# Optimization experiments

Measured on AMD Instinct MI355X. Metric: run time of the kernel, lower is better.

## Reference

```python
import jax, jax.numpy as jnp
import numpy as np

NUM_NODES = 100000
HIDDEN = 128
OFFSET = 2  # GNNEmbedding.OFFSET


def gcn_conv(x, src, dst, W, b, n):
    # GCNConv: D^{-1/2} (A + I) D^{-1/2} X W + b, with self-loops added
    loops = jnp.arange(n)
    s = jnp.concatenate([src, loops])
    d = jnp.concatenate([dst, loops])
    deg = jax.ops.segment_sum(jnp.ones(s.shape, x.dtype), d, num_segments=n)
    dinv = jax.lax.rsqrt(jnp.maximum(deg, 1e-12))
    norm = dinv[s] * dinv[d]          # [E+n]
    msg = x[s] * norm[:, None]        # [E+n, H]  dominant memory traffic
    agg = jax.ops.segment_sum(msg, d, num_segments=n)
    return agg @ W + b


def setup_inputs():
    key = jax.random.key(0)
    ks = jax.random.split(key, 8)
    E = 1_600_000
    B, S = 16, 2048
    src = jax.random.randint(ks[0], (E,), 0, NUM_NODES)
    dst = jax.random.randint(ks[1], (E,), 0, NUM_NODES)
    ei = jnp.stack([src, dst])
    seq = jax.random.randint(ks[2], (B, S), 0, NUM_NODES)
    specials = jax.random.randint(ks[3], (B, S), -2, 20)
    seq = jnp.where(specials < 0, specials, seq)
    emb = jax.random.normal(ks[4], (NUM_NODES + 2, HIDDEN), jnp.float32) * 0.02
    lim = 1.0 / np.sqrt(HIDDEN)
    W0 = jax.random.uniform(ks[5], (HIDDEN, HIDDEN), jnp.float32, -lim, lim)
    W1 = jax.random.uniform(ks[6], (HIDDEN, HIDDEN), jnp.float32, -lim, lim)
    b0 = jnp.zeros((HIDDEN,), jnp.float32)
    b1 = jnp.zeros((HIDDEN,), jnp.float32)
    return {"emb": emb, "W0": W0, "b0": b0, "W1": W1, "b1": b1,
            "ei": ei, "seq": seq}


def reference(emb, W0, b0, W1, b1, ei, seq):
    src, dst = ei[0], ei[1]
    x = emb[:NUM_NODES]                               # embedding(arange(num_nodes))
    h = jax.nn.relu(gcn_conv(x, src, dst, W0, b0, NUM_NODES))
    z = gcn_conv(h, src, dst, W1, b1, NUM_NODES)      # no act on last GCN layer
    nodes = seq >= 0
    node_idx = jnp.where(nodes, seq, 0)
    spec_idx = jnp.where(nodes, 0, seq + OFFSET + NUM_NODES)
    # embs[nodes] = z[seq[nodes]]; embs[~nodes] = emb[seq+OFFSET+num_nodes]
    embs = jnp.where(nodes[..., None], z[node_idx], emb[spec_idx])
    return embs
```

## Files before the change

kernel.cpp:

```cpp
#include <hip/hip_runtime.h>

#define HDIM 128
#define OFF_SPECIAL 2
#define BSTRIDE 48

typedef __attribute__((ext_vector_type(8))) short bf16x8;
typedef __attribute__((ext_vector_type(4))) float f32x4;
typedef __attribute__((ext_vector_type(2))) float f32x2;

__device__ __forceinline__ float bf2f(unsigned short u) {
    union { unsigned int i; float f; } v;
    v.i = ((unsigned int)u) << 16;
    return v.f;
}
__device__ __forceinline__ unsigned short f2bf(float f) {
    union { float f; unsigned int i; } v;
    v.f = f;
    unsigned int x = v.i;
    x += 0x7FFFu + ((x >> 16) & 1u);
    return (unsigned short)(x >> 16);
}

#define XSCALE 16.0f
#define XINV   0.0625f

#define SEG 500
#define PSTRIDE 48
#define PART_W 256
#define CAST_BLOCKS 512
#define FLAG_BLOCKS 16

__global__ void k_part(const int* __restrict__ src, const int* __restrict__ dst,
                       int E, unsigned int* __restrict__ partbuf,
                       int* __restrict__ cntAB, int partN,
                       const float* __restrict__ emb,
                       unsigned char* __restrict__ embf8, int n4,
                       const int* __restrict__ seqp, int P,
                       unsigned char* __restrict__ flag) {
    __shared__ int lcnt[SEG];
    int tid = threadIdx.x;
    if (blockIdx.x < PART_W) {
        for (int i = tid; i < SEG; i += 256) lcnt[i] = 0;
        __syncthreads();
        int w = blockIdx.x;
        int chunk = (E + PART_W - 1) / PART_W;
        int e0 = w * chunk;
        int e1 = e0 + chunk; if (e1 > E) e1 = E;
        for (int e = e0 + tid; e < e1; e += 256) {
            int d = dst[e];
            int s = src[e];
            int seg = d / partN;
            int dloc = d - seg * partN;
            unsigned int pack = (unsigned int)s | ((unsigned int)dloc << 17);
            int slot = atomicAdd(&lcnt[seg], 1);
            if (slot < PSTRIDE)
                partbuf[((size_t)seg * PART_W + w) * PSTRIDE + slot] = pack;
        }
        __syncthreads();
        for (int i = tid; i < SEG; i += 256) {
            int c = lcnt[i];
            cntAB[i * PART_W + w] = c < PSTRIDE ? c : PSTRIDE;
        }
    } else if (blockIdx.x < PART_W + CAST_BLOCKS) {
        int i0 = (blockIdx.x - PART_W) * 256 + tid;
        for (int i = i0; i < n4; i += CAST_BLOCKS * 256) {
            float4 v = ((const float4*)emb)[i];
            int lo = __builtin_amdgcn_cvt_pk_fp8_f32(v.x * XSCALE, v.y * XSCALE, 0, false);
            int pk = __builtin_amdgcn_cvt_pk_fp8_f32(v.z * XSCALE, v.w * XSCALE, lo, true);
            ((int*)embf8)[i] = pk;
        }
    } else {
        int i0 = (blockIdx.x - PART_W - CAST_BLOCKS) * 256 + tid;
        for (int p = i0; p < P; p += FLAG_BLOCKS * 256) {
            int sv = seqp[p];
            if (sv >= 0) flag[sv] = 1;
        }
    }
}

__global__ void k_place(const unsigned int* __restrict__ partbuf,
                        const int* __restrict__ cntAB,
                        int* __restrict__ adjB, int* __restrict__ cnt,
                        float* __restrict__ dinv, int partN, int N) {
    __shared__ int lcur[256];
    int tid = threadIdx.x;
    int s = blockIdx.x;
    for (int i = tid; i < partN; i += 256) lcur[i] = 0;
    __syncthreads();
    int g = tid >> 4;
    int l16 = tid & 15;
    int cpre = cntAB[s * PART_W + g + 16 * l16];
    const unsigned int* segbuf = partbuf + (size_t)s * PART_W * PSTRIDE;
#pragma unroll 4
    for (int k = 0; k < 16; ++k) {
        int c = __shfl(cpre, k, 16);
        int w = g + 16 * k;
        const unsigned int* sb = segbuf + w * PSTRIDE;
        for (int idx = l16; idx < c; idx += 16) {
            unsigned int v = sb[idx];
            int sv = (int)(v & 0x1FFFFu);
            int dloc = (int)(v >> 17);
            int slot = atomicAdd(&lcur[dloc], 1);
            if (slot < BSTRIDE)
                adjB[((size_t)s * partN + dloc) * BSTRIDE + slot] = sv;
        }
    }
    __syncthreads();
    for (int i = tid; i < partN; i += 256) {
        int d = s * partN + i;
        if (d < N) {
            int c = lcur[i];
            cnt[d] = c;
            dinv[d] = rsqrtf((float)c + 1.0f);
        }
    }
}

template <int FP8, int SPARSE>
__global__ __launch_bounds__(256, 8) void k_pull(
        const void* __restrict__ xv, const int* __restrict__ cnt,
        const int* __restrict__ adjB, const float* __restrict__ dinv,
        unsigned short* __restrict__ agg, int N,
        const unsigned char* __restrict__ flag) {
    int row = blockIdx.x * 4 + (threadIdx.x >> 6);
    if (row >= N) return;
    if (SPARSE && !flag[row]) return;
    int lane = threadIdx.x & 63;
    int d = cnt[row];
    if (d > BSTRIDE) d = BSTRIDE;
    const int* nbr = adjB + (size_t)row * BSTRIDE;
    float dr = dinv[row];
    const unsigned char* x8 = (const unsigned char*)xv;
    unsigned int boff = FP8 ? 2u * (unsigned int)lane : 4u * (unsigned int)lane;
    unsigned int rstr = FP8 ? HDIM : HDIM * 2;

    float ax, ay;
    {
        float sc = dr * dr;
        float vx, vy;
        if (FP8) {
            unsigned int p = *(const unsigned short*)(x8 + (size_t)(unsigned)row * rstr + boff);
            f32x2 f = __builtin_amdgcn_cvt_pk_f32_fp8((int)p, false);
            vx = f.x; vy = f.y;
        } else {
            unsigned int u = *(const unsigned int*)(x8 + (size_t)(unsigned)row * rstr + boff);
            vx = bf2f((unsigned short)u); vy = bf2f((unsigned short)(u >> 16));
        }
        ax = vx * sc; ay = vy * sc;
    }
    int t = 0;
    for (; t + 8 <= d; t += 8) {
        int4 q0 = *(const int4*)(nbr + t);
        int4 q1 = *(const int4*)(nbr + t + 4);
        int s[8] = {q0.x, q0.y, q0.z, q0.w, q1.x, q1.y, q1.z, q1.w};
        float nr[8];
        unsigned int u[8];
#pragma unroll
        for (int i = 0; i < 8; ++i) {
            nr[i] = dinv[s[i]] * dr;
            if (FP8) u[i] = *(const unsigned short*)(x8 + (size_t)(unsigned)s[i] * rstr + boff);
            else     u[i] = *(const unsigned int*)(x8 + (size_t)(unsigned)s[i] * rstr + boff);
        }
#pragma unroll
        for (int i = 0; i < 8; ++i) {
            float vx, vy;
            if (FP8) {
                f32x2 f = __builtin_amdgcn_cvt_pk_f32_fp8((int)u[i], false);
                vx = f.x; vy = f.y;
            } else {
                vx = bf2f((unsigned short)u[i]); vy = bf2f((unsigned short)(u[i] >> 16));
            }
            ax = fmaf(vx, nr[i], ax);
            ay = fmaf(vy, nr[i], ay);
        }
    }
    if (t + 4 <= d) {
        int4 q0 = *(const int4*)(nbr + t);
        int s[4] = {q0.x, q0.y, q0.z, q0.w};
        float nr[4];
        unsigned int u[4];
#pragma unroll
        for (int i = 0; i < 4; ++i) {
            nr[i] = dinv[s[i]] * dr;
            if (FP8) u[i] = *(const unsigned short*)(x8 + (size_t)(unsigned)s[i] * rstr + boff);
            else     u[i] = *(const unsigned int*)(x8 + (size_t)(unsigned)s[i] * rstr + boff);
        }
#pragma unroll
        for (int i = 0; i < 4; ++i) {
            float vx, vy;
            if (FP8) {
                f32x2 f = __builtin_amdgcn_cvt_pk_f32_fp8((int)u[i], false);
                vx = f.x; vy = f.y;
            } else {
                vx = bf2f((unsigned short)u[i]); vy = bf2f((unsigned short)(u[i] >> 16));
            }
            ax = fmaf(vx, nr[i], ax);
            ay = fmaf(vy, nr[i], ay);
        }
        t += 4;
    }
    for (; t < d; ++t) {
        int s = nbr[t];
        float nr = dinv[s] * dr;
        float vx, vy;
        if (FP8) {
            unsigned int p = *(const unsigned short*)(x8 + (size_t)(unsigned)s * rstr + boff);
            f32x2 f = __builtin_amdgcn_cvt_pk_f32_fp8((int)p, false);
            vx = f.x; vy = f.y;
        } else {
            unsigned int u = *(const unsigned int*)(x8 + (size_t)(unsigned)s * rstr + boff);
            vx = bf2f((unsigned short)u); vy = bf2f((unsigned short)(u >> 16));
        }
        ax = fmaf(vx, nr, ax);
        ay = fmaf(vy, nr, ay);
    }
    unsigned int pack = (unsigned int)f2bf(ax) | ((unsigned int)f2bf(ay) << 16);
    *(unsigned int*)(agg + (size_t)(unsigned)row * HDIM + 2u * (unsigned int)lane) = pack;
}

template <int RELU, int SPARSE>
__global__ __launch_bounds__(256) void k_gemm_mfma(
        const unsigned short* __restrict__ A, const float* __restrict__ W,
        const float* __restrict__ bias, float bscale,
        unsigned short* __restrict__ out, int N,
        const unsigned char* __restrict__ flag) {
    __shared__ __align__(16) unsigned short Wt[HDIM * 136];
    int tid = threadIdx.x;
    for (int i = tid; i < HDIM * HDIM; i += 256) {
        int k = i >> 7, n = i & 127;
        Wt[n * 136 + k] = f2bf(W[i]);
    }
    int lane = tid & 63;
    int wv = tid >> 6;
    int n15 = lane & 15, q = lane >> 4;
    float bv[8];
#pragma unroll
    for (int ct = 0; ct < 8; ++ct) bv[ct] = bscale * bias[ct * 16 + n15];
    __syncthreads();

    int nChunks = (N + 63) / 64;
    for (int c = blockIdx.x; c < nChunks; c += gridDim.x) {
        int row0 = c * 64 + wv * 16;
        if (SPARSE) {
            int frow = row0 + n15;
            int fl = (frow < N) ? flag[frow] : 0;
            if (__ballot(fl != 0) == 0ULL) continue;
        }
        const unsigned short* arow = A + (size_t)(row0 + n15) * HDIM + q * 8;
        bf16x8 a0 = *(const bf16x8*)(arow);
        bf16x8 a1 = *(const bf16x8*)(arow + 32);
        bf16x8 a2 = *(const bf16x8*)(arow + 64);
        bf16x8 a3 = *(const bf16x8*)(arow + 96);
#pragma unroll
        for (int ct = 0; ct < 8; ++ct) {
            const unsigned short* wrow = &Wt[(ct * 16 + n15) * 136 + q * 8];
            f32x4 acc = {0.f, 0.f, 0.f, 0.f};
            acc = __builtin_amdgcn_mfma_f32_16x16x32_bf16(a0, *(const bf16x8*)(wrow),      acc, 0, 0, 0);
            acc = __builtin_amdgcn_mfma_f32_16x16x32_bf16(a1, *(const bf16x8*)(wrow + 32), acc, 0, 0, 0);
            acc = __builtin_amdgcn_mfma_f32_16x16x32_bf16(a2, *(const bf16x8*)(wrow + 64), acc, 0, 0, 0);
            acc = __builtin_amdgcn_mfma_f32_16x16x32_bf16(a3, *(const bf16x8*)(wrow + 96), acc, 0, 0, 0);
#pragma unroll
            for (int r = 0; r < 4; ++r) {
                int row = row0 + q * 4 + r;
                if (row < N && (!SPARSE || flag[row])) {
                    float v = acc[r] + bv[ct];
                    if (RELU) v = fmaxf(v, 0.0f);
                    out[(size_t)row * HDIM + ct * 16 + n15] = f2bf(v);
                }
            }
        }
    }
}

__global__ void k_gather(const int* __restrict__ seq, int P,
                         const unsigned short* __restrict__ z,
                         const float* __restrict__ emb, int N,
                         float* __restrict__ out) {
    int gid = blockIdx.x * blockDim.x + threadIdx.x;
    int p = gid >> 5, c = gid & 31;
    if (p >= P) return;
    int sv = seq[p];
    float4 v;
    if (sv >= 0) {
        uint2 u = *(const uint2*)(z + (size_t)sv * HDIM + c * 4);
        v = make_float4(bf2f((unsigned short)u.x) * XINV,
                        bf2f((unsigned short)(u.x >> 16)) * XINV,
                        bf2f((unsigned short)u.y) * XINV,
                        bf2f((unsigned short)(u.y >> 16)) * XINV);
    } else {
        v = *(const float4*)(emb + (size_t)(sv + OFF_SPECIAL + N) * HDIM + c * 4);
    }
    *(float4*)(out + (size_t)p * HDIM + c * 4) = v;
}

extern "C" void kernel_launch(void* const* d_in, const int* in_sizes, int n_in,
                              void* d_out, int out_size, void* d_ws, size_t ws_size,
                              hipStream_t stream) {
    const float* emb = (const float*)d_in[0];
    const float* W0  = (const float*)d_in[1];
    const float* b0  = (const float*)d_in[2];
    const float* W1  = (const float*)d_in[3];
    const float* b1  = (const float*)d_in[4];
    const int* ei  = (const int*)d_in[5];
    const int* seq = (const int*)d_in[6];

    int N = in_sizes[0] / HDIM - OFF_SPECIAL;
    int E = in_sizes[5] / 2;
    int P = in_sizes[6];
    const int* srcp = ei;
    const int* dstp = ei + E;

    char* ws = (char*)d_ws;
    size_t off = 0;
    auto alloc = [&](size_t bytes) {
        void* p = ws + off;
        off = (off + bytes + 255) & ~(size_t)255;
        return p;
    };
    unsigned short* aggbf = (unsigned short*)alloc((size_t)N * HDIM * sizeof(unsigned short));
    unsigned short* buf1  = (unsigned short*)alloc((size_t)N * HDIM * sizeof(unsigned short));
    int*   adjB = (int*)alloc((size_t)N * BSTRIDE * sizeof(int));
    int*   cnt  = (int*)alloc((size_t)N * sizeof(int));
    unsigned char* flag = (unsigned char*)alloc((size_t)N);
    float* dinv = (float*)alloc((size_t)N * sizeof(float));
    unsigned int* partbuf = (unsigned int*)aggbf;
    unsigned char* embf8  = (unsigned char*)buf1;
    int* cntAB = (int*)((char*)buf1 + 16u * 1024u * 1024u);

    hipMemsetAsync(flag, 0, (size_t)N, stream);

    int partN = (N + SEG - 1) / SEG;
    int n4 = N * HDIM / 4;
    k_part<<<PART_W + CAST_BLOCKS + FLAG_BLOCKS, 256, 0, stream>>>(
        srcp, dstp, E, partbuf, cntAB, partN, emb, embf8, n4, seq, P, flag);
    k_place<<<SEG, 256, 0, stream>>>(partbuf, cntAB, adjB, cnt, dinv, partN, N);

    int pullBlocks = (N + 3) / 4;

    k_pull<1, 0><<<pullBlocks, 256, 0, stream>>>(embf8, cnt, adjB, dinv, aggbf, N, nullptr);
    k_gemm_mfma<1, 0><<<640, 256, 0, stream>>>(aggbf, W0, b0, XSCALE, buf1, N, nullptr);

    k_pull<0, 1><<<pullBlocks, 256, 0, stream>>>(buf1, cnt, adjB, dinv, aggbf, N, flag);
    k_gemm_mfma<0, 1><<<640, 256, 0, stream>>>(aggbf, W1, b1, XSCALE, aggbf, N, flag);

    k_gather<<<(P * 32 + 255) / 256, 256, 0, stream>>>(seq, P, aggbf, emb, N,
                                                       (float*)d_out);
}
```

Baseline: 307.2 us.

## Fuse first-layer neighbor aggregation with MFMA GEMM and fold flag memset into partition kernel

Adds a k_conv kernel that aggregates 64 rows per block into LDS and then multiplies them by a bf16 copy of W0 with MFMA, with bias and ReLU, in the same kernel. This drops the intermediate aggregation buffer write and read, plus one launch, for layer one. The flag memset moves into k_part, and the flag scatter moves into extra blocks of k_place to remove a separate memset call. The risk is that every block now converts the whole W into LDS, and the fused kernel's large LDS use and 16 serial rows per wave may lower occupancy and latency hiding compared with the separate pull kernel.

New measurement: 384.7 us. 1.25x slower.

```diff
diff --git a/kernel.cpp b/kernel.cpp
--- a/kernel.cpp
+++ b/kernel.cpp
@@ -35,8 +35,7 @@
                        int* __restrict__ cntAB, int partN,
                        const float* __restrict__ emb,
                        unsigned char* __restrict__ embf8, int n4,
-                       const int* __restrict__ seqp, int P,
-                       unsigned char* __restrict__ flag) {
+                       unsigned char* __restrict__ flag, int N) {
     __shared__ int lcnt[SEG];
     int tid = threadIdx.x;
     if (blockIdx.x < PART_W) {
@@ -71,19 +70,31 @@
         }
     } else {
         int i0 = (blockIdx.x - PART_W - CAST_BLOCKS) * 256 + tid;
+        int n16 = N >> 4;
+        for (int i = i0; i < n16; i += FLAG_BLOCKS * 256) {
+            ((int4*)flag)[i] = make_int4(0, 0, 0, 0);
+        }
+        if (blockIdx.x == PART_W + CAST_BLOCKS && tid < (N & 15))
+            flag[(n16 << 4) + tid] = 0;
+    }
+}
+
+__global__ void k_place(const unsigned int* __restrict__ partbuf,
+                        const int* __restrict__ cntAB,
+                        int* __restrict__ adjB, int* __restrict__ cnt,
+                        float* __restrict__ dinv, int partN, int N,
+                        const int* __restrict__ seqp, int P,
+                        unsigned char* __restrict__ flag) {
+    __shared__ int lcur[256];
+    int tid = threadIdx.x;
+    if (blockIdx.x >= SEG) {
+        int i0 = (blockIdx.x - SEG) * 256 + tid;
         for (int p = i0; p < P; p += FLAG_BLOCKS * 256) {
             int sv = seqp[p];
             if (sv >= 0) flag[sv] = 1;
         }
-    }
-}
-
-__global__ void k_place(const unsigned int* __restrict__ partbuf,
-                        const int* __restrict__ cntAB,
-                        int* __restrict__ adjB, int* __restrict__ cnt,
-                        float* __restrict__ dinv, int partN, int N) {
-    __shared__ int lcur[256];
-    int tid = threadIdx.x;
+        return;
+    }
     int s = blockIdx.x;
     for (int i = tid; i < partN; i += 256) lcur[i] = 0;
     __syncthreads();
@@ -116,6 +127,152 @@
     }
 }
 
+template <int FP8, int RELU, int SPARSE>
+__global__ __launch_bounds__(256) void k_conv(
+        const void* __restrict__ xv, const int* __restrict__ cnt,
+        const int* __restrict__ adjB, const float* __restrict__ dinv,
+        const float* __restrict__ W, const float* __restrict__ bias, float bscale,
+        unsigned short* __restrict__ out, int N,
+        const unsigned char* __restrict__ flag) {
+    __shared__ __align__(16) unsigned short Wt[HDIM * 136];
+    __shared__ __align__(16) unsigned short aggT[64 * 136];
+    int tid = threadIdx.x;
+    for (int i = tid; i < HDIM * HDIM; i += 256) {
+        int k = i >> 7, n = i & 127;
+        Wt[n * 136 + k] = f2bf(W[i]);
+    }
+    int lane = tid & 63;
+    int wv = tid >> 6;
+    int n15 = lane & 15, q = lane >> 4;
+    float bv[8];
+#pragma unroll
+    for (int ct = 0; ct < 8; ++ct) bv[ct] = bscale * bias[ct * 16 + n15];
+
+    int row0 = blockIdx.x * 64;
+    const unsigned char* x8 = (const unsigned char*)xv;
+    unsigned int boff = FP8 ? 2u * (unsigned int)lane : 4u * (unsigned int)lane;
+    unsigned int rstr = FP8 ? HDIM : HDIM * 2;
+
+    for (int rr = 0; rr < 16; ++rr) {
+        int lr = wv * 16 + rr;
+        int row = row0 + lr;
+        if (row >= N) break;
+        if (SPARSE && !flag[row]) continue;
+        int d = cnt[row];
+        if (d > BSTRIDE) d = BSTRIDE;
+        const int* nbr = adjB + (size_t)row * BSTRIDE;
+        float dr = dinv[row];
+
+        float ax, ay;
+        {
+            float sc = dr * dr;
+            float vx, vy;
+            if (FP8) {
+                unsigned int p = *(const unsigned short*)(x8 + (size_t)(unsigned)row * rstr + boff);
+                f32x2 f = __builtin_amdgcn_cvt_pk_f32_fp8((int)p, false);
+                vx = f.x; vy = f.y;
+            } else {
+                unsigned int u = *(const unsigned int*)(x8 + (size_t)(unsigned)row * rstr + boff);
+                vx = bf2f((unsigned short)u); vy = bf2f((unsigned short)(u >> 16));
+            }
+            ax = vx * sc; ay = vy * sc;
+        }
+        int t = 0;
+        for (; t + 8 <= d; t += 8) {
+            int4 q0 = *(const int4*)(nbr + t);
+            int4 q1 = *(const int4*)(nbr + t + 4);
+            int s[8] = {q0.x, q0.y, q0.z, q0.w, q1.x, q1.y, q1.z, q1.w};
+            float nr[8];
+            unsigned int u[8];
+#pragma unroll
+            for (int i = 0; i < 8; ++i) {
+                nr[i] = dinv[s[i]] * dr;
+                if (FP8) u[i] = *(const unsigned short*)(x8 + (size_t)(unsigned)s[i] * rstr + boff);
+                else     u[i] = *(const unsigned int*)(x8 + (size_t)(unsigned)s[i] * rstr + boff);
+            }
+#pragma unroll
+            for (int i = 0; i < 8; ++i) {
+                float vx, vy;
+                if (FP8) {
+                    f32x2 f = __builtin_amdgcn_cvt_pk_f32_fp8((int)u[i], false);
+                    vx = f.x; vy = f.y;
+                } else {
+                    vx = bf2f((unsigned short)u[i]); vy = bf2f((unsigned short)(u[i] >> 16));
+                }
+                ax = fmaf(vx, nr[i], ax);
+                ay = fmaf(vy, nr[i], ay);
+            }
+        }
+        if (t + 4 <= d) {
+            int4 q0 = *(const int4*)(nbr + t);
+            int s[4] = {q0.x, q0.y, q0.z, q0.w};
+            float nr[4];
+            unsigned int u[4];
+#pragma unroll
+            for (int i = 0; i < 4; ++i) {
+                nr[i] = dinv[s[i]] * dr;
+                if (FP8) u[i] = *(const unsigned short*)(x8 + (size_t)(unsigned)s[i] * rstr + boff);
+                else     u[i] = *(const unsigned int*)(x8 + (size_t)(unsigned)s[i] * rstr + boff);
+            }
+#pragma unroll
+            for (int i = 0; i < 4; ++i) {
+                float vx, vy;
+                if (FP8) {
+                    f32x2 f = __builtin_amdgcn_cvt_pk_f32_fp8((int)u[i], false);
+                    vx = f.x; vy = f.y;
+                } else {
+                    vx = bf2f((unsigned short)u[i]); vy = bf2f((unsigned short)(u[i] >> 16));
+                }
+                ax = fmaf(vx, nr[i], ax);
+                ay = fmaf(vy, nr[i], ay);
+            }
+            t += 4;
+        }
+        for (; t < d; ++t) {
+            int s = nbr[t];
+            float nr = dinv[s] * dr;
+            float vx, vy;
+            if (FP8) {
+                unsigned int p = *(const unsigned short*)(x8 + (size_t)(unsigned)s * rstr + boff);
+                f32x2 f = __builtin_amdgcn_cvt_pk_f32_fp8((int)p, false);
+                vx = f.x; vy = f.y;
+            } else {
+                unsigned int u = *(const unsigned int*)(x8 + (size_t)(unsigned)s * rstr + boff);
+                vx = bf2f((unsigned short)u); vy = bf2f((unsigned short)(u >> 16));
+            }
+            ax = fmaf(vx, nr, ax);
+            ay = fmaf(vy, nr, ay);
+        }
+        unsigned int pack = (unsigned int)f2bf(ax) | ((unsigned int)f2bf(ay) << 16);
+        *(unsigned int*)(&aggT[lr * 136 + 2 * lane]) = pack;
+    }
+    __syncthreads();
+
+    const unsigned short* arow = &aggT[(wv * 16 + n15) * 136 + q * 8];
+    bf16x8 a0 = *(const bf16x8*)(arow);
+    bf16x8 a1 = *(const bf16x8*)(arow + 32);
+    bf16x8 a2 = *(const bf16x8*)(arow + 64);
+    bf16x8 a3 = *(const bf16x8*)(arow + 96);
+#pragma unroll
+    for (int ct = 0; ct < 8; ++ct) {
+        const unsigned short* wrow = &Wt[(ct * 16 + n15) * 136 + q * 8];
+        f32x4 acc = {0.f, 0.f, 0.f, 0.f};
+        acc = __builtin_amdgcn_mfma_f32_16x16x32_bf16(a0, *(const bf16x8*)(wrow),      acc, 0, 0, 0);
+        acc = __builtin_amdgcn_mfma_f32_16x16x32_bf16(a1, *(const bf16x8*)(wrow + 32), acc, 0, 0, 0);
+        acc = __builtin_amdgcn_mfma_f32_16x16x32_bf16(a2, *(const bf16x8*)(wrow + 64), acc, 0, 0, 0);
+        acc = __builtin_amdgcn_mfma_f32_16x16x32_bf16(a3, *(const bf16x8*)(wrow + 96), acc, 0, 0, 0);
+#pragma unroll
+        for (int r = 0; r < 4; ++r) {
+            int row = row0 + wv * 16 + q * 4 + r;
+            if (row < N && (!SPARSE || flag[row])) {
+                float v = acc[r] + bv[ct];
+                if (RELU) v = fmaxf(v, 0.0f);
+                out[(size_t)row * HDIM + ct * 16 + n15] = f2bf(v);
+            }
+        }
+    }
+}
+
 template <int FP8, int SPARSE>
 __global__ __launch_bounds__(256, 8) void k_pull(
         const void* __restrict__ xv, const int* __restrict__ cnt,
@@ -317,32 +474,31 @@
         off = (off + bytes + 255) & ~(size_t)255;
         return p;
     };
-    unsigned short* aggbf = (unsigned short*)alloc((size_t)N * HDIM * sizeof(unsigned short));
-    unsigned short* buf1  = (unsigned short*)alloc((size_t)N * HDIM * sizeof(unsigned short));
+    unsigned short* bufA = (unsigned short*)alloc((size_t)N * HDIM * sizeof(unsigned short));
+    unsigned short* bufB = (unsigned short*)alloc((size_t)N * HDIM * sizeof(unsigned short));
     int*   adjB = (int*)alloc((size_t)N * BSTRIDE * sizeof(int));
     int*   cnt  = (int*)alloc((size_t)N * sizeof(int));
     unsigned char* flag = (unsigned char*)alloc((size_t)N);
     float* dinv = (float*)alloc((size_t)N * sizeof(float));
-    unsigned int* partbuf = (unsigned int*)aggbf;
-    unsigned char* embf8  = (unsigned char*)buf1;
-    int* cntAB = (int*)((char*)buf1 + 16u * 1024u * 1024u);
-
-    hipMemsetAsync(flag, 0, (size_t)N, stream);
+    unsigned int* partbuf = (unsigned int*)bufA;
+    unsigned char* embf8  = (unsigned char*)bufB;
+    int* cntAB = (int*)((char*)bufB + 16u * 1024u * 1024u);
 
     int partN = (N + SEG - 1) / SEG;
     int n4 = N * HDIM / 4;
     k_part<<<PART_W + CAST_BLOCKS + FLAG_BLOCKS, 256, 0, stream>>>(
-        srcp, dstp, E, partbuf, cntAB, partN, emb, embf8, n4, seq, P, flag);
-    k_place<<<SEG, 256, 0, stream>>>(partbuf, cntAB, adjB, cnt, dinv, partN, N);
+        srcp, dstp, E, partbuf, cntAB, partN, emb, embf8, n4, flag, N);
+    k_place<<<SEG + FLAG_BLOCKS, 256, 0, stream>>>(
+        partbuf, cntAB, adjB, cnt, dinv, partN, N, seq, P, flag);
+
+    int convBlocks = (N + 63) / 64;
+    k_conv<1, 1, 0><<<convBlocks, 256, 0, stream>>>(
+        embf8, cnt, adjB, dinv, W0, b0, XSCALE, bufA, N, nullptr);
 
     int pullBlocks = (N + 3) / 4;
-
-    k_pull<1, 0><<<pullBlocks, 256, 0, stream>>>(embf8, cnt, adjB, dinv, aggbf, N, nullptr);
-    k_gemm_mfma<1, 0><<<640, 256, 0, stream>>>(aggbf, W0, b0, XSCALE, buf1, N, nullptr);
-
-    k_pull<0, 1><<<pullBlocks, 256, 0, stream>>>(buf1, cnt, adjB, dinv, aggbf, N, flag);
-    k_gemm_mfma<0, 1><<<640, 256, 0, stream>>>(aggbf, W1, b1, XSCALE, aggbf, N, flag);
-
-    k_gather<<<(P * 32 + 255) / 256, 256, 0, stream>>>(seq, P, aggbf, emb, N,
+    k_pull<0, 1><<<pullBlocks, 256, 0, stream>>>(bufA, cnt, adjB, dinv, bufB, N, flag);
+    k_gemm_mfma<0, 1><<<640, 256, 0, stream>>>(bufB, W1, b1, XSCALE, bufB, N, flag);
+
+    k_gather<<<(P * 32 + 255) / 256, 256, 0, stream>>>(seq, P, bufB, emb, N,
                                                        (float*)d_out);
 }
```

## Split pull wave into 4 neighbor groups with 16-byte row loads; fold flag memset

Applied to the files above, without the earlier changes.

The aggregation kernel now splits each 64-lane wave into four 16-lane groups. Each group handles a different subset of neighbors and loads 8 features per lane with one wide load, and the partial sums are combined with cross-lane shuffles at the end. This replaces narrow 2/4-byte per-lane gathers with wider vector loads and more neighbors in flight, at the cost of a shuffle reduction and extra registers. The separate flag memset is also removed: the flag buffer is zeroed inside the partition kernel and set in extra blocks of the placement kernel, saving one launch.

Measured after the change: 295.3 us. 1.04x faster.

```diff
diff --git a/kernel.cpp b/kernel.cpp
--- a/kernel.cpp
+++ b/kernel.cpp
@@ -35,8 +35,7 @@
                        int* __restrict__ cntAB, int partN,
                        const float* __restrict__ emb,
                        unsigned char* __restrict__ embf8, int n4,
-                       const int* __restrict__ seqp, int P,
-                       unsigned char* __restrict__ flag) {
+                       unsigned char* __restrict__ flag, int N) {
     __shared__ int lcnt[SEG];
     int tid = threadIdx.x;
     if (blockIdx.x < PART_W) {
@@ -71,19 +70,31 @@
         }
     } else {
         int i0 = (blockIdx.x - PART_W - CAST_BLOCKS) * 256 + tid;
+        int n16 = N >> 4;
+        for (int i = i0; i < n16; i += FLAG_BLOCKS * 256) {
+            ((int4*)flag)[i] = make_int4(0, 0, 0, 0);
+        }
+        if (blockIdx.x == PART_W + CAST_BLOCKS && tid < (N & 15))
+            flag[(n16 << 4) + tid] = 0;
+    }
+}
+
+__global__ void k_place(const unsigned int* __restrict__ partbuf,
+                        const int* __restrict__ cntAB,
+                        int* __restrict__ adjB, int* __restrict__ cnt,
+                        float* __restrict__ dinv, int partN, int N,
+                        const int* __restrict__ seqp, int P,
+                        unsigned char* __restrict__ flag) {
+    __shared__ int lcur[256];
+    int tid = threadIdx.x;
+    if (blockIdx.x >= SEG) {
+        int i0 = (blockIdx.x - SEG) * 256 + tid;
         for (int p = i0; p < P; p += FLAG_BLOCKS * 256) {
             int sv = seqp[p];
             if (sv >= 0) flag[sv] = 1;
         }
-    }
-}
-
-__global__ void k_place(const unsigned int* __restrict__ partbuf,
-                        const int* __restrict__ cntAB,
-                        int* __restrict__ adjB, int* __restrict__ cnt,
-                        float* __restrict__ dinv, int partN, int N) {
-    __shared__ int lcur[256];
-    int tid = threadIdx.x;
+        return;
+    }
     int s = blockIdx.x;
     for (int i = tid; i < partN; i += 256) lcur[i] = 0;
     __syncthreads();
@@ -126,96 +137,126 @@
     if (row >= N) return;
     if (SPARSE && !flag[row]) return;
     int lane = threadIdx.x & 63;
+    int g = lane >> 4, l16 = lane & 15;
     int d = cnt[row];
     if (d > BSTRIDE) d = BSTRIDE;
     const int* nbr = adjB + (size_t)row * BSTRIDE;
     float dr = dinv[row];
     const unsigned char* x8 = (const unsigned char*)xv;
-    unsigned int boff = FP8 ? 2u * (unsigned int)lane : 4u * (unsigned int)lane;
-    unsigned int rstr = FP8 ? HDIM : HDIM * 2;
-
-    float ax, ay;
+    size_t rbytes = FP8 ? HDIM : HDIM * 2;
+    unsigned int boff = (FP8 ? 8u : 16u) * (unsigned int)l16;
+
+    float acc[8];
     {
-        float sc = dr * dr;
-        float vx, vy;
+        float sc = (g == 0) ? dr * dr : 0.0f;
+        const unsigned char* p = x8 + (size_t)(unsigned)row * rbytes + boff;
         if (FP8) {
-            unsigned int p = *(const unsigned short*)(x8 + (size_t)(unsigned)row * rstr + boff);
-            f32x2 f = __builtin_amdgcn_cvt_pk_f32_fp8((int)p, false);
-            vx = f.x; vy = f.y;
+            uint2 u = *(const uint2*)p;
+            f32x2 f0 = __builtin_amdgcn_cvt_pk_f32_fp8((int)u.x, false);
+            f32x2 f1 = __builtin_amdgcn_cvt_pk_f32_fp8((int)u.x, true);
+            f32x2 f2 = __builtin_amdgcn_cvt_pk_f32_fp8((int)u.y, false);
+            f32x2 f3 = __builtin_amdgcn_cvt_pk_f32_fp8((int)u.y, true);
+            acc[0] = f0.x * sc; acc[1] = f0.y * sc;
+            acc[2] = f1.x * sc; acc[3] = f1.y * sc;
+            acc[4] = f2.x * sc; acc[5] = f2.y * sc;
+            acc[6] = f3.x * sc; acc[7] = f3.y * sc;
         } else {
-            unsigned int u = *(const unsigned int*)(x8 + (size_t)(unsigned)row * rstr + boff);
-            vx = bf2f((unsigned short)u); vy = bf2f((unsigned short)(u >> 16));
-        }
-        ax = vx * sc; ay = vy * sc;
-    }
-    int t = 0;
-    for (; t + 8 <= d; t += 8) {
-        int4 q0 = *(const int4*)(nbr + t);
-        int4 q1 = *(const int4*)(nbr + t + 4);
-        int s[8] = {q0.x, q0.y, q0.z, q0.w, q1.x, q1.y, q1.z, q1.w};
-        float nr[8];
-        unsigned int u[8];
+            uint4 u = *(const uint4*)p;
+            acc[0] = bf2f((unsigned short)u.x) * sc;
+            acc[1] = bf2f((unsigned short)(u.x >> 16)) * sc;
+            acc[2] = bf2f((unsigned short)u.y) * sc;
+            acc[3] = bf2f((unsigned short)(u.y >> 16)) * sc;
+            acc[4] = bf2f((unsigned short)u.z) * sc;
+            acc[5] = bf2f((unsigned short)(u.z >> 16)) * sc;
+            acc[6] = bf2f((unsigned short)u.w) * sc;
+            acc[7] = bf2f((unsigned short)(u.w >> 16)) * sc;
+        }
+    }
+    int t = g;
+    for (; t + 4 < d; t += 8) {
+        int s0 = nbr[t], s1 = nbr[t + 4];
+        float n0 = dinv[s0] * dr, n1 = dinv[s1] * dr;
+        const unsigned char* p0 = x8 + (size_t)(unsigned)s0 * rbytes + boff;
+        const unsigned char* p1 = x8 + (size_t)(unsigned)s1 * rbytes + boff;
+        if (FP8) {
+            uint2 a = *(const uint2*)p0;
+            uint2 b = *(const uint2*)p1;
+            f32x2 a0 = __builtin_amdgcn_cvt_pk_f32_fp8((int)a.x, false);
+            f32x2 a1 = __builtin_amdgcn_cvt_pk_f32_fp8((int)a.x, true);
+            f32x2 a2 = __builtin_amdgcn_cvt_pk_f32_fp8((int)a.y, false);
+            f32x2 a3 = __builtin_amdgcn_cvt_pk_f32_fp8((int)a.y, true);
+            acc[0] = fmaf(a0.x, n0, acc[0]); acc[1] = fmaf(a0.y, n0, acc[1]);
+            acc[2] = fmaf(a1.x, n0, acc[2]); acc[3] = fmaf(a1.y, n0, acc[3]);
+            acc[4] = fmaf(a2.x, n0, acc[4]); acc[5] = fmaf(a2.y, n0, acc[5]);
+            acc[6] = fmaf(a3.x, n0, acc[6]); acc[7] = fmaf(a3.y, n0, acc[7]);
+            f32x2 b0 = __builtin_amdgcn_cvt_pk_f32_fp8((int)b.x, false);
+            f32x2 b1 = __builtin_amdgcn_cvt_pk_f32_fp8((int)b.x, true);
+            f32x2 b2 = __builtin_amdgcn_cvt_pk_f32_fp8((int)b.y, false);
+            f32x2 b3 = __builtin_amdgcn_cvt_pk_f32_fp8((int)b.y, true);
+            acc[0] = fmaf(b0.x, n1, acc[0]); acc[1] = fmaf(b0.y, n1, acc[1]);
+            acc[2] = fmaf(b1.x, n1, acc[2]); acc[3] = fmaf(b1.y, n1, acc[3]);
+            acc[4] = fmaf(b2.x, n1, acc[4]); acc[5] = fmaf(b2.y, n1, acc[5]);
+            acc[6] = fmaf(b3.x, n1, acc[6]); acc[7] = fmaf(b3.y, n1, acc[7]);
+        } else {
+            uint4 a = *(const uint4*)p0;
+            uint4 b = *(const uint4*)p1;
+            acc[0] = fmaf(bf2f((unsigned short)a.x),         n0, acc[0]);
+            acc[1] = fmaf(bf2f((unsigned short)(a.x >> 16)), n0, acc[1]);
+            acc[2] = fmaf(bf2f((unsigned short)a.y),         n0, acc[2]);
+            acc[3] = fmaf(bf2f((unsigned short)(a.y >> 16)), n0, acc[3]);
+            acc[4] = fmaf(bf2f((unsigned short)a.z),         n0, acc[4]);
+            acc[5] = fmaf(bf2f((unsigned short)(a.z >> 16)), n0, acc[5]);
+            acc[6] = fmaf(bf2f((unsigned short)a.w),         n0, acc[6]);
+            acc[7] = fmaf(bf2f((unsigned short)(a.w >> 16)), n0, acc[7]);
+            acc[0] = fmaf(bf2f((unsigned short)b.x),         n1, acc[0]);
+            acc[1] = fmaf(bf2f((unsigned short)(b.x >> 16)), n1, acc[1]);
+            acc[2] = fmaf(bf2f((unsigned short)b.y),         n1, acc[2]);
+            acc[3] = fmaf(bf2f((unsigned short)(b.y >> 16)), n1, acc[3]);
+            acc[4] = fmaf(bf2f((unsigned short)b.z),         n1, acc[4]);
+            acc[5] = fmaf(bf2f((unsigned short)(b.z >> 16)), n1, acc[5]);
+            acc[6] = fmaf(bf2f((unsigned short)b.w),         n1, acc[6]);
+            acc[7] = fmaf(bf2f((unsigned short)(b.w >> 16)), n1, acc[7]);
+        }
+    }
+    if (t < d) {
+        int s0 = nbr[t];
+        float n0 = dinv[s0] * dr;
+        const unsigned char* p0 = x8 + (size_t)(unsigned)s0 * rbytes + boff;
+        if (FP8) {
+            uint2 a = *(const uint2*)p0;
+            f32x2 a0 = __builtin_amdgcn_cvt_pk_f32_fp8((int)a.x, false);
+            f32x2 a1 = __builtin_amdgcn_cvt_pk_f32_fp8((int)a.x, true);
+            f32x2 a2 = __builtin_amdgcn_cvt_pk_f32_fp8((int)a.y, false);
+            f32x2 a3 = __builtin_amdgcn_cvt_pk_f32_fp8((int)a.y, true);
+            acc[0] = fmaf(a0.x, n0, acc[0]); acc[1] = fmaf(a0.y, n0, acc[1]);
+            acc[2] = fmaf(a1.x, n0, acc[2]); acc[3] = fmaf(a1.y, n0, acc[3]);
+            acc[4] = fmaf(a2.x, n0, acc[4]); acc[5] = fmaf(a2.y, n0, acc[5]);
+            acc[6] = fmaf(a3.x, n0, acc[6]); acc[7] = fmaf(a3.y, n0, acc[7]);
+        } else {
+            uint4 a = *(const uint4*)p0;
+            acc[0] = fmaf(bf2f((unsigned short)a.x),         n0, acc[0]);
+            acc[1] = fmaf(bf2f((unsigned short)(a.x >> 16)), n0, acc[1]);
+            acc[2] = fmaf(bf2f((unsigned short)a.y),         n0, acc[2]);
+            acc[3] = fmaf(bf2f((unsigned short)(a.y >> 16)), n0, acc[3]);
+            acc[4] = fmaf(bf2f((unsigned short)a.z),         n0, acc[4]);
+            acc[5] = fmaf(bf2f((unsigned short)(a.z >> 16)), n0, acc[5]);
+            acc[6] = fmaf(bf2f((unsigned short)a.w),         n0, acc[6]);
+            acc[7] = fmaf(bf2f((unsigned short)(a.w >> 16)), n0, acc[7]);
+        }
+    }
 #pragma unroll
-        for (int i = 0; i < 8; ++i) {
-            nr[i] = dinv[s[i]] * dr;
-            if (FP8) u[i] = *(const unsigned short*)(x8 + (size_t)(unsigned)s[i] * rstr + boff);
-            else     u[i] = *(const unsigned int*)(x8 + (size_t)(unsigned)s[i] * rstr + boff);
-        }
-#pragma unroll
-        for (int i = 0; i < 8; ++i) {
-            float vx, vy;
-            if (FP8) {
-                f32x2 f = __builtin_amdgcn_cvt_pk_f32_fp8((int)u[i], false);
-                vx = f.x; vy = f.y;
-            } else {
-                vx = bf2f((unsigned short)u[i]); vy = bf2f((unsigned short)(u[i] >> 16));
-            }
-            ax = fmaf(vx, nr[i], ax);
-            ay = fmaf(vy, nr[i], ay);
-        }
-    }
-    if (t + 4 <= d) {
-        int4 q0 = *(const int4*)(nbr + t);
-        int s[4] = {q0.x, q0.y, q0.z, q0.w};
-        float nr[4];
-        unsigned int u[4];
-#pragma unroll
-        for (int i = 0; i < 4; ++i) {
-            nr[i] = dinv[s[i]] * dr;
-            if (FP8) u[i] = *(const unsigned short*)(x8 + (size_t)(unsigned)s[i] * rstr + boff);
-            else     u[i] = *(const unsigned int*)(x8 + (size_t)(unsigned)s[i] * rstr + boff);
-        }
-#pragma unroll
-        for (int i = 0; i < 4; ++i) {
-            float vx, vy;
-            if (FP8) {
-                f32x2 f = __builtin_amdgcn_cvt_pk_f32_fp8((int)u[i], false);
-                vx = f.x; vy = f.y;
-            } else {
-                vx = bf2f((unsigned short)u[i]); vy = bf2f((unsigned short)(u[i] >> 16));
-            }
-            ax = fmaf(vx, nr[i], ax);
-            ay = fmaf(vy, nr[i], ay);
-        }
-        t += 4;
-    }
-    for (; t < d; ++t) {
-        int s = nbr[t];
-        float nr = dinv[s] * dr;
-        float vx, vy;
-        if (FP8) {
-            unsigned int p = *(const unsigned short*)(x8 + (size_t)(unsigned)s * rstr + boff);
-            f32x2 f = __builtin_amdgcn_cvt_pk_f32_fp8((int)p, false);
-            vx = f.x; vy = f.y;
-        } else {
-            unsigned int u = *(const unsigned int*)(x8 + (size_t)(unsigned)s * rstr + boff);
-            vx = bf2f((unsigned short)u); vy = bf2f((unsigned short)(u >> 16));
-        }
-        ax = fmaf(vx, nr, ax);
-        ay = fmaf(vy, nr, ay);
-    }
-    unsigned int pack = (unsigned int)f2bf(ax) | ((unsigned int)f2bf(ay) << 16);
-    *(unsigned int*)(agg + (size_t)(unsigned)row * HDIM + 2u * (unsigned int)lane) = pack;
+    for (int i = 0; i < 8; ++i) {
+        acc[i] += __shfl_xor(acc[i], 16);
+        acc[i] += __shfl_xor(acc[i], 32);
+    }
+    if (g == 0) {
+        unsigned int w0 = (unsigned int)f2bf(acc[0]) | ((unsigned int)f2bf(acc[1]) << 16);
+        unsigned int w1 = (unsigned int)f2bf(acc[2]) | ((unsigned int)f2bf(acc[3]) << 16);
+        unsigned int w2 = (unsigned int)f2bf(acc[4]) | ((unsigned int)f2bf(acc[5]) << 16);
+        unsigned int w3 = (unsigned int)f2bf(acc[6]) | ((unsigned int)f2bf(acc[7]) << 16);
+        uint4 o = make_uint4(w0, w1, w2, w3);
+        *(uint4*)(agg + (size_t)(unsigned)row * HDIM + 8u * (unsigned int)l16) = o;
+    }
 }
 
 template <int RELU, int SPARSE>
@@ -327,13 +368,12 @@
     unsigned char* embf8  = (unsigned char*)buf1;
     int* cntAB = (int*)((char*)buf1 + 16u * 1024u * 1024u);
 
-    hipMemsetAsync(flag, 0, (size_t)N, stream);
-
     int partN = (N + SEG - 1) / SEG;
     int n4 = N * HDIM / 4;
     k_part<<<PART_W + CAST_BLOCKS + FLAG_BLOCKS, 256, 0, stream>>>(
-        srcp, dstp, E, partbuf, cntAB, partN, emb, embf8, n4, seq, P, flag);
-    k_place<<<SEG, 256, 0, stream>>>(partbuf, cntAB, adjB, cnt, dinv, partN, N);
+        srcp, dstp, E, partbuf, cntAB, partN, emb, embf8, n4, flag, N);
+    k_place<<<SEG + FLAG_BLOCKS, 256, 0, stream>>>(
+        partbuf, cntAB, adjB, cnt, dinv, partN, N, seq, P, flag);
 
     int pullBlocks = (N + 3) / 4;
 
```
